# Kernel tuning notes

Hardware: AMD Instinct MI355X
Metric: run time of the kernel (lower is better)

Reference implementation:

```python
import jax, jax.numpy as jnp
import numpy as np

NB, T, NS, NC = 32, 256, 64, 32
NSC = NS + NC


def setup_inputs() -> dict:
    key = jax.random.key(0)
    k1, k2, k3, k4, k5, k6 = jax.random.split(key, 6)
    Qr = jax.random.normal(k1, (NB, T, NSC, NSC), jnp.float32)
    # SPD cost matrices (example does Q = Q.mT @ Q); add ridge so Quu is well conditioned
    Q = jnp.einsum('btki,btkj->btij', Qr, Qr) / NSC + 0.5 * jnp.eye(NSC, dtype=jnp.float32)
    p = jax.random.normal(k2, (NB, T, NSC), jnp.float32)
    A = jnp.eye(NS, dtype=jnp.float32)[None] + 0.01 * jax.random.normal(k3, (NB, NS, NS), jnp.float32)
    B = 0.1 * jax.random.normal(k4, (NB, NS, NC), jnp.float32)
    c1 = 0.01 * jax.random.normal(k5, (NB, NS), jnp.float32)
    x_init = jax.random.normal(k6, (NB, NS), jnp.float32)
    return {'Q': Q, 'p': p, 'A': A, 'B': B, 'c1': c1, 'x_init': x_init}


def _lqr(Q, p, A, B, c1, x_init):
    ns = A.shape[-1]
    F = jnp.concatenate([A, B], axis=-1)  # [nb, ns, nsc]

    # ---- backward Riccati recursion (t = T-1 .. 0) ----
    def bwd(carry, inp):
        V, v = carry              # [nb,ns,ns], [nb,ns]
        Qt, pt = inp              # [nb,nsc,nsc], [nb,nsc]
        FtV = jnp.einsum('bsj,bsk->bjk', F, V)          # F^T V  [nb,nsc,ns]
        Qh = Qt + FtV @ F                               # Q + F^T V F
        qh = pt + jnp.einsum('bjk,bk->bj', FtV, c1) + jnp.einsum('bsj,bs->bj', F, v)
        Qxx = Qh[:, :ns, :ns]
        Qxu = Qh[:, :ns, ns:]
        Qux = Qh[:, ns:, :ns]
        Quu = Qh[:, ns:, ns:]
        qx, qu = qh[:, :ns], qh[:, ns:]
        K = -jnp.linalg.solve(Quu, Qux)                 # -Quu^{-1} Qux  [nb,nc,ns]
        kk = -jnp.linalg.solve(Quu, qu[..., None])[..., 0]
        Kt = jnp.swapaxes(K, -1, -2)
        Vn = Qxx + Qxu @ K + Kt @ Qux + Kt @ (Quu @ K)
        vn = qx + jnp.einsum('bsu,bu->bs', Qxu, kk) \
            + jnp.einsum('bus,bu->bs', K, qu + jnp.einsum('buw,bw->bu', Quu, kk))
        return (Vn, vn), (K, kk)

    nb = Q.shape[0]
    V0 = jnp.zeros((nb, ns, ns), Q.dtype)
    v0 = jnp.zeros((nb, ns), Q.dtype)
    Qs = jnp.swapaxes(Q, 0, 1)   # [T,nb,nsc,nsc]
    ps = jnp.swapaxes(p, 0, 1)
    _, (Ks, ks) = jax.lax.scan(bwd, (V0, v0), (jnp.flip(Qs, 0), jnp.flip(ps, 0)))
    Ks = jnp.flip(Ks, 0)
    ks = jnp.flip(ks, 0)

    # ---- forward rollout (t = 0 .. T-1) ----
    def fwd(x, inp):
        K, kk, Qt, pt = inp
        u = jnp.einsum('bus,bs->bu', K, x) + kk
        tau = jnp.concatenate([x, u], axis=-1)
        c = 0.5 * jnp.einsum('bi,bij,bj->b', tau, Qt, tau) + jnp.einsum('bi,bi->b', pt, tau)
        xn = jnp.einsum('bij,bj->bi', A, x) + jnp.einsum('bij,bj->bi', B, u) + c1
        return xn, (x, u, c)

    _, (xs, us, cs) = jax.lax.scan(fwd, x_init, (Ks, ks, Qs, ps))
    x = jnp.swapaxes(xs, 0, 1)   # [nb,T,ns]
    u = jnp.swapaxes(us, 0, 1)   # [nb,T,nc]
    cost = jnp.sum(cs, axis=0)   # [nb]
    return x, u, cost


def reference(Q, p, A, B, c1, x_init):
    return _lqr(Q, p, A, B, c1, x_init)
```

## Files before the change

### kernel.cpp

```cpp
#include <hip/hip_runtime.h>

#define NB 32
#define T 256
#define NS 64
#define NC 32
#define NSC 96

typedef short bf16x8 __attribute__((ext_vector_type(8)));
typedef float f32x4  __attribute__((ext_vector_type(4)));

#define COMP(v,i) ((i)==0?(v).x:((i)==1?(v).y:((i)==2?(v).z:(v).w)))

static __device__ __forceinline__ float dot4(float4 a, float4 b){
    return fmaf(a.x,b.x, fmaf(a.y,b.y, fmaf(a.z,b.z, a.w*b.w)));
}
static __device__ __forceinline__ unsigned short f2bf(float x){
    unsigned int u = __float_as_uint(x);
    u += 0x7FFFu + ((u >> 16) & 1u);
    return (unsigned short)(u >> 16);
}
static __device__ __forceinline__ float bf2f(unsigned short h){
    return __uint_as_float(((unsigned int)h) << 16);
}

__device__ __align__(16) float g_KtG[(size_t)NB*T*NS*NC];
__device__ __align__(16) float g_kkG[(size_t)NB*T*NC];

#define BROW 72
#define SR32 36

__device__ __forceinline__ void p2geom(int tix, int& i0, int& j0, int& osel){
    if (tix < 16)      { i0 = (tix & 3)*16;              j0 = (tix >> 2)*16;        osel = 0; }
    else if (tix < 24) { const int q = tix-16; i0 = (q & 3)*16;  j0 = 64 + (q >> 2)*16; osel = 1; }
    else               { const int q = tix-24; i0 = 64 + (q & 1)*16; j0 = 64 + (q >> 1)*16; osel = 2; }
}

#define P1TILE(tix) { \
    const int s0 = ((tix) & 3) * 16, j0 = ((tix) >> 2) * 16; \
    f32x4 c = {0.f, 0.f, 0.f, 0.f}; \
    _Pragma("unroll") \
    for (int kc = 0; kc < 2; ++kc) { \
        const int ch = (kc*4 + lk) * 8; \
        const bf16x8 ah = *(const bf16x8*)&Vbh[(s0+lm)*BROW + ch]; \
        const bf16x8 al = *(const bf16x8*)&Vbl[(s0+lm)*BROW + ch]; \
        const bf16x8 bh = *(const bf16x8*)&Fth[(j0+lm)*BROW + ch]; \
        const bf16x8 bl = *(const bf16x8*)&Ftl[(j0+lm)*BROW + ch]; \
        c = __builtin_amdgcn_mfma_f32_16x16x32_bf16(ah, bh, c, 0, 0, 0); \
        c = __builtin_amdgcn_mfma_f32_16x16x32_bf16(ah, bl, c, 0, 0, 0); \
        c = __builtin_amdgcn_mfma_f32_16x16x32_bf16(al, bh, c, 0, 0, 0); \
    } \
    ushort4 hv, lv; float rm_; \
    hv.x = f2bf(c[0]); rm_ = c[0] - bf2f(hv.x); lv.x = f2bf(rm_); \
    hv.y = f2bf(c[1]); rm_ = c[1] - bf2f(hv.y); lv.y = f2bf(rm_); \
    hv.z = f2bf(c[2]); rm_ = c[2] - bf2f(hv.z); lv.z = f2bf(rm_); \
    hv.w = f2bf(c[3]); rm_ = c[3] - bf2f(hv.w); lv.w = f2bf(rm_); \
    const int ui = (j0+lm)*BROW + s0 + lk*4; \
    *(ushort4*)&Wth[ui] = hv; \
    *(ushort4*)&Wtl[ui] = lv; \
}

#define P2TILE(cin, tix) { \
    int i0_, j0_, os_; p2geom((tix), i0_, j0_, os_); \
    f32x4 c = cin; \
    _Pragma("unroll") \
    for (int kc = 0; kc < 2; ++kc) { \
        const int ch = (kc*4 + lk) * 8; \
        const bf16x8 ah = *(const bf16x8*)&Fth[(i0_+lm)*BROW + ch]; \
        const bf16x8 al = *(const bf16x8*)&Ftl[(i0_+lm)*BROW + ch]; \
        const bf16x8 bh = *(const bf16x8*)&Wth[(j0_+lm)*BROW + ch]; \
        const bf16x8 bl = *(const bf16x8*)&Wtl[(j0_+lm)*BROW + ch]; \
        c = __builtin_amdgcn_mfma_f32_16x16x32_bf16(ah, bh, c, 0, 0, 0); \
        c = __builtin_amdgcn_mfma_f32_16x16x32_bf16(ah, bl, c, 0, 0, 0); \
        c = __builtin_amdgcn_mfma_f32_16x16x32_bf16(al, bh, c, 0, 0, 0); \
    } \
    _Pragma("unroll") \
    for (int r = 0; r < 4; ++r) { \
        const int i_ = i0_ + lk*4 + r, j_ = j0_ + lm; \
        if (os_ == 0) { V[i_][j_] = c[r]; } \
        else if (os_ == 1) { \
            const int u_ = j_ - 64; \
            Qxu[i_][u_] = c[r]; \
            const unsigned short h_ = f2bf(c[r]); \
            Qxuh[i_*SR32 + u_] = h_; \
            Qxul[i_*SR32 + u_] = f2bf(c[r] - bf2f(h_)); \
        } else { \
            const int wr_ = i_ - 64, u_ = j_ - 64; \
            Maug[wr_][u_] = c[r]; QuuC[wr_][u_] = c[r]; \
            const unsigned short h_ = f2bf(c[r]); \
            Quuh[wr_*SR32 + u_] = h_; \
            Quul[wr_*SR32 + u_] = f2bf(c[r] - bf2f(h_)); \
            if (wr_ == 0) { prow[0][u_] = c[r]; prow[0][32+u_] = (u_ == 0) ? 1.f : 0.f; } \
            if (u_ == 0) pfac[0][wr_] = c[r]; \
        } \
    } \
}

__global__ __launch_bounds__(512)
void lqr_bwd(const float* __restrict__ Qg_, const float* __restrict__ pg_,
             const float* __restrict__ Ag_, const float* __restrict__ Bg_,
             const float* __restrict__ c1g_, const float* __restrict__ x0g_,
             float* __restrict__ outc)
{
    __shared__ __align__(16) float V[64][68];
    __shared__ __align__(16) unsigned short Vbh[64*BROW];
    __shared__ __align__(16) unsigned short Vbl[64*BROW];
    __shared__ __align__(16) unsigned short Fth[96*BROW];
    __shared__ __align__(16) unsigned short Ftl[96*BROW];
    __shared__ __align__(16) unsigned short Wth[96*BROW];
    __shared__ __align__(16) unsigned short Wtl[96*BROW];
    __shared__ __align__(16) float Qxu[64][36];
    __shared__ __align__(16) float QuuC[32][36];
    __shared__ __align__(16) float Maug[32][68];
    __shared__ __align__(16) float prow[2][64];
    __shared__ __align__(16) float pfac[2][32];
    __shared__ __align__(16) unsigned short Qxuh[64*SR32], Qxul[64*SR32];
    __shared__ __align__(16) unsigned short Kth[64*SR32],  Ktl[64*SR32];
    __shared__ __align__(16) unsigned short Minvh[32*SR32], Minvl[32*SR32];
    __shared__ __align__(16) unsigned short Quuh[32*SR32],  Quul[32*SR32];
    __shared__ __align__(16) unsigned short Rth[64*SR32];
    __shared__ __align__(16) float qh[96];
    __shared__ __align__(16) float gv[64];
    __shared__ __align__(16) float hbuf[32];
    __shared__ __align__(16) float c1l[64];
    __shared__ __align__(16) float vl[64];
    __shared__ __align__(16) float kkl[32];
    __shared__ __align__(16) float x0l[64];
    __shared__ float wpart[8];
    __shared__ float wAcc;

    const int tid = threadIdx.x;
    const int b   = blockIdx.x;
    const int w   = tid >> 6;
    const int lm  = tid & 15;
    const int lk  = (tid & 63) >> 4;

    const float* Qg = Qg_ + (size_t)b*T*NSC*NSC;
    const float* pg = pg_ + (size_t)b*T*NSC;
    const float* Ag = Ag_ + (size_t)b*NS*NS;
    const float* Bg = Bg_ + (size_t)b*NS*NC;
    float* KtG = g_KtG + (size_t)b*T*NS*NC;
    float* kkG = g_kkG + (size_t)b*T*NC;

    for (int e = tid; e < 96*64; e += 512) {
        const int j = e >> 6, s = e & 63;
        const float x = (j < 64) ? Ag[s*64 + j] : Bg[s*32 + (j-64)];
        const unsigned short h = f2bf(x);
        Fth[j*BROW + s] = h;
        Ftl[j*BROW + s] = f2bf(x - bf2f(h));
    }
    for (int e = tid; e < 64*BROW; e += 512) { Vbh[e] = 0; Vbl[e] = 0; }
    for (int e = tid; e < 64*68; e += 512) ((float*)V)[e] = 0.f;
    if (tid < 64) { c1l[tid] = c1g_[b*64+tid]; vl[tid] = 0.f; x0l[tid] = x0g_[b*64+tid]; }
    if (tid == 0) wAcc = 0.f;
    __syncthreads();

    const int wq  = tid >> 4;
    const int gjq = tid & 15, gj0 = gjq * 4;

    const int p2s = (w < 4) ? w*4 : 16 + (w-4)*3;
    const int p2n = (w < 4) ? 4 : 3;

    for (int t = T-1; t >= 0; --t) {
        const float* Qt = Qg + (size_t)t*NSC*NSC;
        const float* pt = pg + (size_t)t*NSC;

        f32x4 qt0, qt1, qt2, qt3;
        {
            int i0, j0, os;
            p2geom(p2s+0, i0, j0, os);
            const float* s0p = Qt + (size_t)(i0 + lk*4)*96 + j0 + lm;
            qt0[0]=s0p[0]; qt0[1]=s0p[96]; qt0[2]=s0p[192]; qt0[3]=s0p[288];
            p2geom(p2s+1, i0, j0, os);
            const float* s1p = Qt + (size_t)(i0 + lk*4)*96 + j0 + lm;
            qt1[0]=s1p[0]; qt1[1]=s1p[96]; qt1[2]=s1p[192]; qt1[3]=s1p[288];
            p2geom(p2s+2, i0, j0, os);
            const float* s2p = Qt + (size_t)(i0 + lk*4)*96 + j0 + lm;
            qt2[0]=s2p[0]; qt2[1]=s2p[96]; qt2[2]=s2p[192]; qt2[3]=s2p[288];
            if (p2n == 4) {
                p2geom(p2s+3, i0, j0, os);
                const float* s3p = Qt + (size_t)(i0 + lk*4)*96 + j0 + lm;
                qt3[0]=s3p[0]; qt3[1]=s3p[96]; qt3[2]=s3p[192]; qt3[3]=s3p[288];
            } else { qt3 = qt0; }
        }

        {
            const int l = tid >> 3, g = tid & 7;
            const int k0 = g * 8;
            float d = dot4(*(const float4*)&V[l][k0],   *(const float4*)&c1l[k0])
                    + dot4(*(const float4*)&V[l][k0+4], *(const float4*)&c1l[k0+4]);
            d += __shfl_xor(d, 1); d += __shfl_xor(d, 2); d += __shfl_xor(d, 4);
            if (g == 0) gv[l] = d + vl[l];
            float term = (g == 0) ? c1l[l]*(0.5f*d + vl[l]) : 0.f;
            term += __shfl_xor(term, 8); term += __shfl_xor(term, 16); term += __shfl_xor(term, 32);
            if ((tid & 63) == 0) wpart[w] = term;
        }
        __syncthreads();

        if (tid < 384) {
            const int j = tid >> 2, g = tid & 3;
            const int s0 = g * 16;
            const bf16x8 h0 = *(const bf16x8*)&Fth[j*BROW + s0];
            const bf16x8 l0 = *(const bf16x8*)&Ftl[j*BROW + s0];
            const bf16x8 h1 = *(const bf16x8*)&Fth[j*BROW + s0 + 8];
            const bf16x8 l1 = *(const bf16x8*)&Ftl[j*BROW + s0 + 8];
            float s = 0.f;
            #pragma unroll
            for (int i = 0; i < 8; ++i) {
                s = fmaf(bf2f((unsigned short)h0[i]) + bf2f((unsigned short)l0[i]), gv[s0+i],   s);
                s = fmaf(bf2f((unsigned short)h1[i]) + bf2f((unsigned short)l1[i]), gv[s0+8+i], s);
            }
            s += __shfl_xor(s, 1); s += __shfl_xor(s, 2);
            if (g == 0) qh[j] = pt[j] + s;
        } else if (tid == 448) {
            float s = 0.f;
            #pragma unroll
            for (int i = 0; i < 8; ++i) s += wpart[i];
            wAcc += s;
        }
        __syncthreads();

        {
            const int st = w * 3;
            P1TILE(st+0)
            P1TILE(st+1)
            P1TILE(st+2)
        }
        __syncthreads();

        P2TILE(qt0, p2s+0)
        P2TILE(qt1, p2s+1)
        P2TILE(qt2, p2s+2)
        if (p2n == 4) { P2TILE(qt3, p2s+3) }
        __syncthreads();

        {
            float4 m;
            if (gjq < 8) m = *(const float4*)&Maug[wq][gj0];
            else {
                const int base = gj0 - 32;
                m.x = (base+0==wq)?1.f:0.f; m.y = (base+1==wq)?1.f:0.f;
                m.z = (base+2==wq)?1.f:0.f; m.w = (base+3==wq)?1.f:0.f;
            }
            #pragma unroll
            for (int k = 0; k < 32; ++k) {
                const int par = k & 1, nxt = par ^ 1;
                const float pinv = 1.0f / prow[par][k];
                const float4 pr = *(const float4*)&prow[par][gj0];
                if (wq == k) {
                    m.x = pr.x*pinv; m.y = pr.y*pinv; m.z = pr.z*pinv; m.w = pr.w*pinv;
                } else {
                    const float fac = pfac[par][wq]*pinv;
                    m.x = fmaf(-fac,pr.x,m.x); m.y = fmaf(-fac,pr.y,m.y);
                    m.z = fmaf(-fac,pr.z,m.z); m.w = fmaf(-fac,pr.w,m.w);
                }
                if (k < 31) {
                    if (wq == k+1) *(float4*)&prow[nxt][gj0] = m;
                    if (((k+1)>>2) == gjq) pfac[nxt][wq] = COMP(m,(k+1)&3);
                } else if (gjq >= 8) {
                    *(float4*)&Maug[wq][gj0] = m;
                }
                __syncthreads();
            }
        }

        {
            const int e0 = tid * 2;
            const int u = e0 >> 5, w0 = e0 & 31;
            const float m0 = Maug[u][32+w0], m1 = Maug[u][32+w0+1];
            const unsigned short h0 = f2bf(m0), h1 = f2bf(m1);
            Minvh[u*SR32 + w0]   = h0;  Minvl[u*SR32 + w0]   = f2bf(m0 - bf2f(h0));
            Minvh[u*SR32 + w0+1] = h1;  Minvl[u*SR32 + w0+1] = f2bf(m1 - bf2f(h1));
        }
        __syncthreads();

        {
            const int i0 = (w & 3)*16, u0 = (w >> 2)*16;
            const int ch = lk*8;
            f32x4 c = {0.f,0.f,0.f,0.f};
            const bf16x8 ah = *(const bf16x8*)&Qxuh[(i0+lm)*SR32 + ch];
            const bf16x8 al = *(const bf16x8*)&Qxul[(i0+lm)*SR32 + ch];
            const bf16x8 bh = *(const bf16x8*)&Minvh[(u0+lm)*SR32 + ch];
            const bf16x8 bl = *(const bf16x8*)&Minvl[(u0+lm)*SR32 + ch];
            c = __builtin_amdgcn_mfma_f32_16x16x32_bf16(ah, bh, c, 0, 0, 0);
            c = __builtin_amdgcn_mfma_f32_16x16x32_bf16(ah, bl, c, 0, 0, 0);
            c = __builtin_amdgcn_mfma_f32_16x16x32_bf16(al, bh, c, 0, 0, 0);
            #pragma unroll
            for (int r = 0; r < 4; ++r) {
                const int i_ = i0 + lk*4 + r, u_ = u0 + lm;
                const float kv = -c[r];
                KtG[(size_t)t*2048 + i_*32 + u_] = kv;
                const unsigned short h = f2bf(kv);
                Kth[i_*SR32 + u_] = h;
                Ktl[i_*SR32 + u_] = f2bf(kv - bf2f(h));
            }
            if (tid < 32) {
                float ka = 0.f;
                #pragma unroll
                for (int w4 = 0; w4 < 8; ++w4)
                    ka -= dot4(*(const float4*)&Maug[tid][32+w4*4], *(const float4*)&qh[64+w4*4]);
                kkl[tid] = ka;
                kkG[t*32 + tid] = ka;
            }
        }
        __syncthreads();

        {
            const int j0 = (w & 3)*16, u0 = (w >> 2)*16;
            const int ch = lk*8;
            f32x4 c;
            #pragma unroll
            for (int r = 0; r < 4; ++r) c[r] = Qxu[j0 + lk*4 + r][u0 + lm];
            const bf16x8 ah = *(const bf16x8*)&Kth[(j0+lm)*SR32 + ch];
            const bf16x8 al = *(const bf16x8*)&Ktl[(j0+lm)*SR32 + ch];
            const bf16x8 bh = *(const bf16x8*)&Quuh[(u0+lm)*SR32 + ch];
            const bf16x8 bl = *(const bf16x8*)&Quul[(u0+lm)*SR32 + ch];
            c = __builtin_amdgcn_mfma_f32_16x16x32_bf16(ah, bh, c, 0, 0, 0);
            c = __builtin_amdgcn_mfma_f32_16x16x32_bf16(ah, bl, c, 0, 0, 0);
            c = __builtin_amdgcn_mfma_f32_16x16x32_bf16(al, bh, c, 0, 0, 0);
            #pragma unroll
            for (int r = 0; r < 4; ++r)
                Rth[(j0 + lk*4 + r)*SR32 + u0 + lm] = f2bf(c[r]);
            if (tid < 32) {
                float h = qh[64+tid];
                #pragma unroll
                for (int w4 = 0; w4 < 8; ++w4)
                    h += dot4(*(const float4*)&QuuC[tid][w4*4], *(const float4*)&kkl[w4*4]);
                hbuf[tid] = h;
            }
        }
        __syncthreads();

        #pragma unroll
        for (int half = 0; half < 2; ++half) {
            const int tx = w + half*8;
            const int i0 = (tx & 3)*16, j0 = (tx >> 2)*16;
            const int ch = lk*8;
            f32x4 c;
            #pragma unroll
            for (int r = 0; r < 4; ++r) c[r] = V[i0 + lk*4 + r][j0 + lm];
            const bf16x8 ah  = *(const bf16x8*)&Qxuh[(i0+lm)*SR32 + ch];
            const bf16x8 al  = *(const bf16x8*)&Qxul[(i0+lm)*SR32 + ch];
            const bf16x8 bh  = *(const bf16x8*)&Kth[(j0+lm)*SR32 + ch];
            const bf16x8 bl  = *(const bf16x8*)&Ktl[(j0+lm)*SR32 + ch];
            const bf16x8 a2h = *(const bf16x8*)&Kth[(i0+lm)*SR32 + ch];
            const bf16x8 b2h = *(const bf16x8*)&Rth[(j0+lm)*SR32 + ch];
            c = __builtin_amdgcn_mfma_f32_16x16x32_bf16(ah,  bh,  c, 0, 0, 0);
            c = __builtin_amdgcn_mfma_f32_16x16x32_bf16(ah,  bl,  c, 0, 0, 0);
            c = __builtin_amdgcn_mfma_f32_16x16x32_bf16(al,  bh,  c, 0, 0, 0);
            c = __builtin_amdgcn_mfma_f32_16x16x32_bf16(a2h, b2h, c, 0, 0, 0);
            #pragma unroll
            for (int r = 0; r < 4; ++r) V[i0 + lk*4 + r][j0 + lm] = c[r];
        }
        __syncthreads();

        if (tid < 256) {
            const int a = tid >> 4, bq = tid & 15;
            if (a < bq) {
                float4 t1[4], t2[4];
                #pragma unroll
                for (int r = 0; r < 4; ++r) {
                    t1[r] = *(const float4*)&V[4*a+r][4*bq];
                    t2[r] = *(const float4*)&V[4*bq+r][4*a];
                }
                #pragma unroll
                for (int r = 0; r < 4; ++r) {
                    float4 o, p;
                    o.x = 0.5f*(COMP(t1[r],0)+COMP(t2[0],r));
                    o.y = 0.5f*(COMP(t1[r],1)+COMP(t2[1],r));
                    o.z = 0.5f*(COMP(t1[r],2)+COMP(t2[2],r));
                    o.w = 0.5f*(COMP(t1[r],3)+COMP(t2[3],r));
                    p.x = 0.5f*(COMP(t2[r],0)+COMP(t1[0],r));
                    p.y = 0.5f*(COMP(t2[r],1)+COMP(t1[1],r));
                    p.z = 0.5f*(COMP(t2[r],2)+COMP(t1[2],r));
                    p.w = 0.5f*(COMP(t2[r],3)+COMP(t1[3],r));
                    *(float4*)&V[4*a+r][4*bq] = o;
                    *(float4*)&V[4*bq+r][4*a] = p;
                    ushort4 oh, ol, ph, pl;
                    oh.x=f2bf(o.x); ol.x=f2bf(o.x-bf2f(oh.x));
                    oh.y=f2bf(o.y); ol.y=f2bf(o.y-bf2f(oh.y));
                    oh.z=f2bf(o.z); ol.z=f2bf(o.z-bf2f(oh.z));
                    oh.w=f2bf(o.w); ol.w=f2bf(o.w-bf2f(oh.w));
                    ph.x=f2bf(p.x); pl.x=f2bf(p.x-bf2f(ph.x));
                    ph.y=f2bf(p.y); pl.y=f2bf(p.y-bf2f(ph.y));
                    ph.z=f2bf(p.z); pl.z=f2bf(p.z-bf2f(ph.z));
                    ph.w=f2bf(p.w); pl.w=f2bf(p.w-bf2f(ph.w));
                    *(ushort4*)&Vbh[(4*a+r)*BROW + 4*bq] = oh;
                    *(ushort4*)&Vbl[(4*a+r)*BROW + 4*bq] = ol;
                    *(ushort4*)&Vbh[(4*bq+r)*BROW + 4*a] = ph;
                    *(ushort4*)&Vbl[(4*bq+r)*BROW + 4*a] = pl;
                }
            } else if (a == bq) {
                float4 t1[4];
                #pragma unroll
                for (int r = 0; r < 4; ++r) t1[r] = *(const float4*)&V[4*a+r][4*a];
                #pragma unroll
                for (int r = 0; r < 4; ++r) {
                    float4 o;
                    o.x = 0.5f*(COMP(t1[r],0)+COMP(t1[0],r));
                    o.y = 0.5f*(COMP(t1[r],1)+COMP(t1[1],r));
                    o.z = 0.5f*(COMP(t1[r],2)+COMP(t1[2],r));
                    o.w = 0.5f*(COMP(t1[r],3)+COMP(t1[3],r));
                    *(float4*)&V[4*a+r][4*a] = o;
                    ushort4 oh, ol;
                    oh.x=f2bf(o.x); ol.x=f2bf(o.x-bf2f(oh.x));
                    oh.y=f2bf(o.y); ol.y=f2bf(o.y-bf2f(oh.y));
                    oh.z=f2bf(o.z); ol.z=f2bf(o.z-bf2f(oh.z));
                    oh.w=f2bf(o.w); ol.w=f2bf(o.w-bf2f(oh.w));
                    *(ushort4*)&Vbh[(4*a+r)*BROW + 4*a] = oh;
                    *(ushort4*)&Vbl[(4*a+r)*BROW + 4*a] = ol;
                }
            }
        } else if (tid < 320) {
            const int l = tid - 256;
            float vv = qh[l];
            #pragma unroll
            for (int u4 = 0; u4 < 8; ++u4)
                vv += dot4(*(const float4*)&Qxu[l][u4*4], *(const float4*)&kkl[u4*4]);
            #pragma unroll
            for (int cg = 0; cg < 4; ++cg) {
                const bf16x8 h8 = *(const bf16x8*)&Kth[l*SR32 + cg*8];
                const bf16x8 l8 = *(const bf16x8*)&Ktl[l*SR32 + cg*8];
                #pragma unroll
                for (int i = 0; i < 8; ++i)
                    vv = fmaf(bf2f((unsigned short)h8[i]) + bf2f((unsigned short)l8[i]),
                              hbuf[cg*8+i], vv);
            }
            vl[l] = vv;
        } else if (tid < 352) {
            const int u = tid - 320;
            float r = kkl[u]*(hbuf[u] + qh[64+u]);
            r += __shfl_xor(r,16); r += __shfl_xor(r,8); r += __shfl_xor(r,4);
            r += __shfl_xor(r,2);  r += __shfl_xor(r,1);
            if (u == 0) wAcc += 0.5f*r;
        }
        __syncthreads();
    }

    if (tid < 64) {
        float rd = 0.f;
        #pragma unroll
        for (int k4 = 0; k4 < 16; ++k4)
            rd += dot4(*(const float4*)&V[tid][k4*4], *(const float4*)&x0l[k4*4]);
        float ps = x0l[tid]*(0.5f*rd + vl[tid]);
        ps += __shfl_xor(ps,32); ps += __shfl_xor(ps,16); ps += __shfl_xor(ps,8);
        ps += __shfl_xor(ps,4);  ps += __shfl_xor(ps,2);  ps += __shfl_xor(ps,1);
        if (tid == 0) outc[b] = wAcc + ps;
    }
}

__global__ __launch_bounds__(256)
void lqr_fwd(const float* __restrict__ Ag_, const float* __restrict__ Bg_,
             const float* __restrict__ c1g_, const float* __restrict__ x0g_,
             float* __restrict__ outx, float* __restrict__ outu)
{
    __shared__ __align__(16) float At[64][68];
    __shared__ __align__(16) float Bt[32][68];
    __shared__ __align__(16) float KtL[64][36];
    __shared__ float xl[64], ul[32], cl[64], kl[32], xnb[64];

    const int tid = threadIdx.x;
    const int b = blockIdx.x;

    const float* KtG = g_KtG + (size_t)b*T*NS*NC;
    const float* kkG = g_kkG + (size_t)b*T*NC;

    for (int e = tid; e < NS*NS; e += 256) At[e&63][e>>6] = Ag_[(size_t)b*4096 + e];
    for (int e = tid; e < NS*NC; e += 256) Bt[e&31][e>>5] = Bg_[(size_t)b*2048 + e];
    if (tid < 64) { xl[tid] = x0g_[b*64 + tid]; cl[tid] = c1g_[b*64 + tid]; }

    {
        const int i1 = tid*4, i2 = 1024 + tid*4;
        const float4 a = *(const float4*)&KtG[i1];
        const float4 c = *(const float4*)&KtG[i2];
        *(float4*)&KtL[i1>>5][i1&31] = a;
        *(float4*)&KtL[i2>>5][i2&31] = c;
        if (tid < 32) kl[tid] = kkG[tid];
    }
    __syncthreads();

    float4 g0, g1; float kn = 0.f;
    for (int t = 0; t < T; ++t) {
        if (t+1 < T) {
            g0 = *(const float4*)&KtG[(size_t)(t+1)*2048 + tid*4];
            g1 = *(const float4*)&KtG[(size_t)(t+1)*2048 + 1024 + tid*4];
            if (tid < 32) kn = kkG[(t+1)*32 + tid];
        }

        if (tid < 64) outx[((size_t)b*T + t)*64 + tid] = xl[tid];
        if (tid < 128) {
            const int u = tid >> 2, sp = tid & 3, s0 = sp*16;
            float r = 0.f;
            #pragma unroll
            for (int i = 0; i < 16; ++i) r = fmaf(KtL[s0+i][u], xl[s0+i], r);
            r += __shfl_xor(r, 1); r += __shfl_xor(r, 2);
            if (sp == 0) {
                const float uu = r + kl[u];
                ul[u] = uu;
                outu[((size_t)b*T + t)*32 + u] = uu;
            }
        }
        __syncthreads();

        {
            const int o = tid >> 2, sp = tid & 3;
            float r = 0.f;
            #pragma unroll
            for (int i = 0; i < 16; ++i) { const int j = sp*16 + i; r = fmaf(At[j][o], xl[j], r); }
            #pragma unroll
            for (int i = 0; i < 8; ++i)  { const int w2 = sp*8 + i; r = fmaf(Bt[w2][o], ul[w2], r); }
            r += __shfl_xor(r, 1); r += __shfl_xor(r, 2);
            if (sp == 0) xnb[o] = r + cl[o];
        }
        __syncthreads();

        if (tid < 64) xl[tid] = xnb[tid];
        if (t+1 < T) {
            const int i1 = tid*4, i2 = 1024 + tid*4;
            *(float4*)&KtL[i1>>5][i1&31] = g0;
            *(float4*)&KtL[i2>>5][i2&31] = g1;
            if (tid < 32) kl[tid] = kn;
        }
        __syncthreads();
    }
}

extern "C" void kernel_launch(void* const* d_in, const int* in_sizes, int n_in,
                              void* d_out, int out_size, void* d_ws, size_t ws_size,
                              hipStream_t stream)
{
    const float* Q  = (const float*)d_in[0];
    const float* p  = (const float*)d_in[1];
    const float* A  = (const float*)d_in[2];
    const float* B  = (const float*)d_in[3];
    const float* c1 = (const float*)d_in[4];
    const float* x0 = (const float*)d_in[5];

    float* outx = (float*)d_out;
    float* outu = outx + (size_t)NB*T*NS;
    float* outc = outu + (size_t)NB*T*NC;

    lqr_bwd<<<NB, 512, 0, stream>>>(Q, p, A, B, c1, x0, outc);
    lqr_fwd<<<NB, 256, 0, stream>>>(A, B, c1, x0, outx, outu);
}
```

Baseline: 4.916 ms.

## Block Gauss-Jordan pivots by two and overlap qh computation with P1 tiles

The 32-step Gauss-Jordan inversion of Quu now eliminates two pivots per step using an explicit 2x2 block inverse, which halves the number of barrier-separated iterations. The qh/gv computation is moved onto a dedicated eighth wave that runs concurrently with the P1 MFMA tiles on the other seven waves. Two barriers go away as a result, and the bf16 hi/lo split of Minv is folded into the final elimination step, removing one more pass. In exchange the 2x2 pivoting adds arithmetic per step, may change numerical stability, and leaves the P1 work spread unevenly across waves.

```diff
diff --git a/kernel.cpp b/kernel.cpp
--- a/kernel.cpp
+++ b/kernel.cpp
@@ -89,8 +89,8 @@
             const unsigned short h_ = f2bf(c[r]); \
             Quuh[wr_*SR32 + u_] = h_; \
             Quul[wr_*SR32 + u_] = f2bf(c[r] - bf2f(h_)); \
-            if (wr_ == 0) { prow[0][u_] = c[r]; prow[0][32+u_] = (u_ == 0) ? 1.f : 0.f; } \
-            if (u_ == 0) pfac[0][wr_] = c[r]; \
+            if (wr_ < 2) prow2[0][wr_][u_] = c[r]; \
+            if (u_ < 2)  pfac2[0][u_][wr_] = c[r]; \
         } \
     } \
 }
@@ -111,8 +111,8 @@
     __shared__ __align__(16) float Qxu[64][36];
     __shared__ __align__(16) float QuuC[32][36];
     __shared__ __align__(16) float Maug[32][68];
-    __shared__ __align__(16) float prow[2][64];
-    __shared__ __align__(16) float pfac[2][32];
+    __shared__ __align__(16) float prow2[2][2][64];
+    __shared__ __align__(16) float pfac2[2][2][32];
     __shared__ __align__(16) unsigned short Qxuh[64*SR32], Qxul[64*SR32];
     __shared__ __align__(16) unsigned short Kth[64*SR32],  Ktl[64*SR32];
     __shared__ __align__(16) unsigned short Minvh[32*SR32], Minvl[32*SR32];
@@ -125,7 +125,6 @@
     __shared__ __align__(16) float vl[64];
     __shared__ __align__(16) float kkl[32];
     __shared__ __align__(16) float x0l[64];
-    __shared__ float wpart[8];
     __shared__ float wAcc;
 
     const int tid = threadIdx.x;
@@ -183,47 +182,44 @@
             } else { qt3 = qt0; }
         }
 
-        {
-            const int l = tid >> 3, g = tid & 7;
-            const int k0 = g * 8;
-            float d = dot4(*(const float4*)&V[l][k0],   *(const float4*)&c1l[k0])
-                    + dot4(*(const float4*)&V[l][k0+4], *(const float4*)&c1l[k0+4]);
-            d += __shfl_xor(d, 1); d += __shfl_xor(d, 2); d += __shfl_xor(d, 4);
-            if (g == 0) gv[l] = d + vl[l];
-            float term = (g == 0) ? c1l[l]*(0.5f*d + vl[l]) : 0.f;
-            term += __shfl_xor(term, 8); term += __shfl_xor(term, 16); term += __shfl_xor(term, 32);
-            if ((tid & 63) == 0) wpart[w] = term;
-        }
-        __syncthreads();
-
-        if (tid < 384) {
-            const int j = tid >> 2, g = tid & 3;
-            const int s0 = g * 16;
-            const bf16x8 h0 = *(const bf16x8*)&Fth[j*BROW + s0];
-            const bf16x8 l0 = *(const bf16x8*)&Ftl[j*BROW + s0];
-            const bf16x8 h1 = *(const bf16x8*)&Fth[j*BROW + s0 + 8];
-            const bf16x8 l1 = *(const bf16x8*)&Ftl[j*BROW + s0 + 8];
-            float s = 0.f;
-            #pragma unroll
-            for (int i = 0; i < 8; ++i) {
-                s = fmaf(bf2f((unsigned short)h0[i]) + bf2f((unsigned short)l0[i]), gv[s0+i],   s);
-                s = fmaf(bf2f((unsigned short)h1[i]) + bf2f((unsigned short)l1[i]), gv[s0+8+i], s);
-            }
-            s += __shfl_xor(s, 1); s += __shfl_xor(s, 2);
-            if (g == 0) qh[j] = pt[j] + s;
-        } else if (tid == 448) {
-            float s = 0.f;
-            #pragma unroll
-            for (int i = 0; i < 8; ++i) s += wpart[i];
-            wAcc += s;
-        }
-        __syncthreads();
-
-        {
-            const int st = w * 3;
+        if (w < 7) {
+            const int st = (w < 3) ? w*4 : 12 + (w-3)*3;
             P1TILE(st+0)
             P1TILE(st+1)
             P1TILE(st+2)
+            if (w < 3) { P1TILE(st+3) }
+        } else {
+            const int ll = tid & 63;
+            float d = 0.f;
+            #pragma unroll
+            for (int k4 = 0; k4 < 16; ++k4)
+                d += dot4(*(const float4*)&V[ll][k4*4], *(const float4*)&c1l[k4*4]);
+            gv[ll] = d + vl[ll];
+            float ps = c1l[ll]*(0.5f*d + vl[ll]);
+            ps += __shfl_xor(ps,32); ps += __shfl_xor(ps,16); ps += __shfl_xor(ps,8);
+            ps += __shfl_xor(ps,4);  ps += __shfl_xor(ps,2);  ps += __shfl_xor(ps,1);
+            if (ll == 0) wAcc += ps;
+            float q0 = pt[ll];
+            float q1 = (ll < 32) ? pt[64+ll] : 0.f;
+            #pragma unroll
+            for (int cg = 0; cg < 8; ++cg) {
+                const bf16x8 h1 = *(const bf16x8*)&Fth[ll*BROW + cg*8];
+                const bf16x8 l1 = *(const bf16x8*)&Ftl[ll*BROW + cg*8];
+                bf16x8 h2 = h1, l2 = l1;
+                if (ll < 32) {
+                    h2 = *(const bf16x8*)&Fth[(64+ll)*BROW + cg*8];
+                    l2 = *(const bf16x8*)&Ftl[(64+ll)*BROW + cg*8];
+                }
+                #pragma unroll
+                for (int i = 0; i < 8; ++i) {
+                    const float gs = gv[cg*8 + i];
+                    q0 = fmaf(bf2f((unsigned short)h1[i]) + bf2f((unsigned short)l1[i]), gs, q0);
+                    if (ll < 32)
+                        q1 = fmaf(bf2f((unsigned short)h2[i]) + bf2f((unsigned short)l2[i]), gs, q1);
+                }
+            }
+            qh[ll] = q0;
+            if (ll < 32) qh[64+ll] = q1;
         }
         __syncthreads();
 
@@ -231,6 +227,10 @@
         P2TILE(qt1, p2s+1)
         P2TILE(qt2, p2s+2)
         if (p2n == 4) { P2TILE(qt3, p2s+3) }
+        if (tid < 64) {
+            const int rr = tid >> 5, cc2 = tid & 31;
+            prow2[0][rr][32 + cc2] = (cc2 == rr) ? 1.f : 0.f;
+        }
         __syncthreads();
 
         {
@@ -242,36 +242,56 @@
                 m.z = (base+2==wq)?1.f:0.f; m.w = (base+3==wq)?1.f:0.f;
             }
             #pragma unroll
-            for (int k = 0; k < 32; ++k) {
-                const int par = k & 1, nxt = par ^ 1;
-                const float pinv = 1.0f / prow[par][k];
-                const float4 pr = *(const float4*)&prow[par][gj0];
+            for (int blk = 0; blk < 16; ++blk) {
+                const int k = blk*2;
+                const int par = blk & 1, nxt = par ^ 1;
+                const float a  = prow2[par][0][k],  bq = prow2[par][0][k+1];
+                const float cc = prow2[par][1][k],  d  = prow2[par][1][k+1];
+                const float idet = 1.0f / fmaf(a, d, -bq*cc);
+                const float4 r0 = *(const float4*)&prow2[par][0][gj0];
+                const float4 r1 = *(const float4*)&prow2[par][1][gj0];
                 if (wq == k) {
-                    m.x = pr.x*pinv; m.y = pr.y*pinv; m.z = pr.z*pinv; m.w = pr.w*pinv;
+                    m.x = (d*r0.x - bq*r1.x)*idet;
+                    m.y = (d*r0.y - bq*r1.y)*idet;
+                    m.z = (d*r0.z - bq*r1.z)*idet;
+                    m.w = (d*r0.w - bq*r1.w)*idet;
+                } else if (wq == k+1) {
+                    m.x = (a*r1.x - cc*r0.x)*idet;
+                    m.y = (a*r1.y - cc*r0.y)*idet;
+                    m.z = (a*r1.z - cc*r0.z)*idet;
+                    m.w = (a*r1.w - cc*r0.w)*idet;
                 } else {
-                    const float fac = pfac[par][wq]*pinv;
-                    m.x = fmaf(-fac,pr.x,m.x); m.y = fmaf(-fac,pr.y,m.y);
-                    m.z = fmaf(-fac,pr.z,m.z); m.w = fmaf(-fac,pr.w,m.w);
-                }
-                if (k < 31) {
-                    if (wq == k+1) *(float4*)&prow[nxt][gj0] = m;
-                    if (((k+1)>>2) == gjq) pfac[nxt][wq] = COMP(m,(k+1)&3);
-                } else if (gjq >= 8) {
-                    *(float4*)&Maug[wq][gj0] = m;
+                    const float C0 = pfac2[par][0][wq], C1 = pfac2[par][1][wq];
+                    const float E0 = (C0*d - C1*cc)*idet;
+                    const float E1 = (C1*a - C0*bq)*idet;
+                    m.x = fmaf(-E0, r0.x, fmaf(-E1, r1.x, m.x));
+                    m.y = fmaf(-E0, r0.y, fmaf(-E1, r1.y, m.y));
+                    m.z = fmaf(-E0, r0.z, fmaf(-E1, r1.z, m.z));
+                    m.w = fmaf(-E0, r0.w, fmaf(-E1, r1.w, m.w));
+                }
+                if (blk < 15) {
+                    if (wq == k+2)      *(float4*)&prow2[nxt][0][gj0] = m;
+                    else if (wq == k+3) *(float4*)&prow2[nxt][1][gj0] = m;
+                    if (gjq == ((k+2) >> 2)) {
+                        pfac2[nxt][0][wq] = COMP(m, (k+2)&3);
+                        pfac2[nxt][1][wq] = COMP(m, (k+3)&3);
+                    }
                 }
                 __syncthreads();
             }
-        }
-
-        {
-            const int e0 = tid * 2;
-            const int u = e0 >> 5, w0 = e0 & 31;
-            const float m0 = Maug[u][32+w0], m1 = Maug[u][32+w0+1];
-            const unsigned short h0 = f2bf(m0), h1 = f2bf(m1);
-            Minvh[u*SR32 + w0]   = h0;  Minvl[u*SR32 + w0]   = f2bf(m0 - bf2f(h0));
-            Minvh[u*SR32 + w0+1] = h1;  Minvl[u*SR32 + w0+1] = f2bf(m1 - bf2f(h1));
-        }
-        __syncthreads();
+            if (gjq >= 8) {
+                *(float4*)&Maug[wq][gj0] = m;
+                ushort4 hv, lv;
+                hv.x = f2bf(m.x); lv.x = f2bf(m.x - bf2f(hv.x));
+                hv.y = f2bf(m.y); lv.y = f2bf(m.y - bf2f(hv.y));
+                hv.z = f2bf(m.z); lv.z = f2bf(m.z - bf2f(hv.z));
+                hv.w = f2bf(m.w); lv.w = f2bf(m.w - bf2f(hv.w));
+                const int u_ = gj0 - 32;
+                *(ushort4*)&Minvh[wq*SR32 + u_] = hv;
+                *(ushort4*)&Minvl[wq*SR32 + u_] = lv;
+            }
+            __syncthreads();
+        }
 
         {
             const int i0 = (w & 3)*16, u0 = (w >> 2)*16;
```

Result: slower. 6.273 ms (+27.6%).
